# Performance work log

Hardware: AMD Instinct MI355X
Metric: run time of the kernel (lower is better)

Reference implementation:

```python
import jax, jax.numpy as jnp
import numpy as np

E = 8       # num experts
T = 1024    # num tokens
H = 1024    # hidden dim
I = 1024    # intermediate dim (per gate/up half)


def setup_inputs() -> dict:
    key = jax.random.key(0)
    k1, k2, k3, k4 = jax.random.split(key, 4)
    return {
        "hidden_states": jax.random.normal(k1, (T, H), jnp.float32),
        "router_logits": jax.random.normal(k2, (T, E), jnp.float32),
        # W13 stored pre-transposed as in the module: [E, H, 2*I]
        "W13": jax.random.normal(k3, (E, H, 2 * I), jnp.float32) * 0.02,
        # W2 stored pre-transposed: [E, I, H]
        "W2": jax.random.normal(k4, (E, I, H), jnp.float32) * 0.02,
        "top_k": 2,
    }


def reference(hidden_states, router_logits, W13, W2, top_k):
    num_experts = router_logits.shape[-1]
    # --- routing: topk_softmax (softmax over all experts, then top-k) ---
    probs = jax.nn.softmax(router_logits, axis=-1)            # [T, E]
    w, idx = jax.lax.top_k(probs, top_k)                      # [T, K]
    # renormalize=True path of moe_gather
    w = w / jnp.sum(w, axis=-1, keepdims=True)
    # combine weights per expert: [T, E]
    combine = jnp.sum(jax.nn.one_hot(idx, num_experts, dtype=w.dtype) * w[..., None], axis=1)
    # --- grouped gate-up GEMM + silu_and_mul ---
    h13 = jnp.einsum('th,ehf->tef', hidden_states, W13)       # [T, E, 2I]
    gate, up = jnp.split(h13, 2, axis=-1)                     # each [T, E, I]
    act = jax.nn.silu(gate) * up                              # silu_and_mul
    # --- grouped down GEMM ---
    down = jnp.einsum('tei,eih->teh', act, W2)                # [T, E, H]
    # --- combine (moe_gather) ---
    return jnp.einsum('te,teh->th', combine, down)            # [T, H]
```

## Files before the change

kernel.cpp:

```cpp
#include <hip/hip_runtime.h>
#include <hip/hip_bf16.h>
#include <stdint.h>

#define NE    8
#define NTOK  1024
#define NH    1024
#define NI    1024
#define N13   2048
#define NPAIR 2048

typedef __attribute__((ext_vector_type(8))) short short8;
typedef __attribute__((ext_vector_type(4))) float f32x4;
typedef unsigned short u16;
typedef unsigned int   u32;

#define WAIT_VM4 0x0F74
#define WAIT_VM3 0x0F73
#define WAIT_VM0 0x0F70

__device__ __forceinline__ u16 f2bf(float x) {
    union { float f; u32 u; } v; v.f = x;
    return (u16)((v.u + 0x7fffu + ((v.u >> 16) & 1u)) >> 16);
}

__device__ __forceinline__ void async_ld16(u16* lds, const u16* g) {
    __builtin_amdgcn_global_load_lds(
        (const __attribute__((address_space(1))) u32*)g,
        (__attribute__((address_space(3))) u32*)lds, 16, 0, 0);
}

__global__ __launch_bounds__(256) void route_kernel(
    const float* __restrict__ logits,
    int* __restrict__ counts, int* __restrict__ pair_tok,
    float* __restrict__ pair_w)
{
    __shared__ int s_cnt[NE];
    __shared__ int s_base[NE];
    const int tid = threadIdx.x;
    if (tid < NE) s_cnt[tid] = 0;
    __syncthreads();

    int eA[4][2]; int slotA[4][2]; float wA[4][2];

    #pragma unroll
    for (int i = 0; i < 4; i++) {
        const int t = tid * 4 + i;
        float l[NE];
        #pragma unroll
        for (int e = 0; e < NE; e++) l[e] = logits[t * NE + e];
        int i0 = 0;
        #pragma unroll
        for (int e = 1; e < NE; e++) if (l[e] > l[i0]) i0 = e;
        int i1 = -1;
        #pragma unroll
        for (int e = 0; e < NE; e++) {
            if (e == i0) continue;
            if (i1 < 0 || l[e] > l[i1]) i1 = e;
        }
        const float e10 = __expf(l[i1] - l[i0]);
        const float inv = 1.0f / (1.0f + e10);
        eA[i][0] = i0; eA[i][1] = i1;
        wA[i][0] = inv; wA[i][1] = e10 * inv;
        slotA[i][0] = atomicAdd(&s_cnt[i0], 1);
        slotA[i][1] = atomicAdd(&s_cnt[i1], 1);
    }
    __syncthreads();
    if (tid == 0) {
        int acc = 0;
        #pragma unroll
        for (int e = 0; e < NE; e++) { s_base[e] = acc; acc += s_cnt[e]; }
    }
    __syncthreads();
    if (tid < NE) counts[tid] = s_cnt[tid];
    #pragma unroll
    for (int i = 0; i < 4; i++) {
        const int t = tid * 4 + i;
        #pragma unroll
        for (int k = 0; k < 2; k++) {
            const int p = s_base[eA[i][k]] + slotA[i][k];
            pair_tok[p] = t;
            pair_w[p]   = wA[i][k];
        }
    }
}

__device__ __forceinline__ bool find_tile(
    const int* __restrict__ counts, int tile, int bm, int ntn,
    int& e_o, int& mt_o, int& nt_o, int& cnt_o, int& base_o)
{
    int base = 0;
    #pragma unroll
    for (int e = 0; e < NE; e++) {
        const int cnt = counts[e];
        const int mtiles = (cnt + bm - 1) / bm;
        const int tiles = mtiles * ntn;
        if (tile < tiles) {
            e_o = e; mt_o = tile / ntn; nt_o = tile - (tile / ntn) * ntn;
            cnt_o = cnt; base_o = base; return true;
        }
        tile -= tiles; base += cnt;
    }
    return false;
}

__global__ __launch_bounds__(256) void cvt_x_kernel(
    const float* __restrict__ src, u16* __restrict__ dst)
{
    const int i = blockIdx.x * 256 + threadIdx.x;
    const float4* s = (const float4*)src;
    const float4 a = s[2 * i], b = s[2 * i + 1];
    uint4 o;
    o.x = f2bf(a.x) | ((u32)f2bf(a.y) << 16);
    o.y = f2bf(a.z) | ((u32)f2bf(a.w) << 16);
    o.z = f2bf(b.x) | ((u32)f2bf(b.y) << 16);
    o.w = f2bf(b.z) | ((u32)f2bf(b.w) << 16);
    *(uint4*)(dst + (size_t)i * 8) = o;
}

__global__ __launch_bounds__(256) void cvt_tr_kernel(
    const float* __restrict__ src, u16* __restrict__ dst, int K, int N)
{
    __shared__ float Ts[64][65];
    const int ktiles = K >> 6, ntiles = N >> 6;
    const int tpe = ktiles * ntiles;
    const int e = blockIdx.x / tpe;
    const int rem = blockIdx.x - e * tpe;
    const int kt = rem / ntiles, nt = rem - (rem / ntiles) * ntiles;
    const float* sb = src + ((size_t)e * K + (size_t)kt * 64) * N + nt * 64;
    const int tid = threadIdx.x;

    #pragma unroll
    for (int i = 0; i < 4; i++) {
        const int idx = tid + i * 256;
        const int r = idx >> 4, c = (idx & 15) << 2;
        const float4 v = *(const float4*)(sb + (size_t)r * N + c);
        Ts[r][c + 0] = v.x; Ts[r][c + 1] = v.y;
        Ts[r][c + 2] = v.z; Ts[r][c + 3] = v.w;
    }
    __syncthreads();
    u16* db = dst + ((size_t)e * N + (size_t)nt * 64) * K + kt * 64;
    #pragma unroll
    for (int i = 0; i < 2; i++) {
        const int u = tid + i * 256;
        const int n = u >> 3, k8 = (u & 7) << 3;
        uint4 o;
        o.x = f2bf(Ts[k8 + 0][n]) | ((u32)f2bf(Ts[k8 + 1][n]) << 16);
        o.y = f2bf(Ts[k8 + 2][n]) | ((u32)f2bf(Ts[k8 + 3][n]) << 16);
        o.z = f2bf(Ts[k8 + 4][n]) | ((u32)f2bf(Ts[k8 + 5][n]) << 16);
        o.w = f2bf(Ts[k8 + 6][n]) | ((u32)f2bf(Ts[k8 + 7][n]) << 16);
        *(uint4*)(db + (size_t)n * K + k8) = o;
    }
}

__global__ __launch_bounds__(256) void gemm1_kernel(
    const u16* __restrict__ Xb, const u16* __restrict__ W13t,
    const int* __restrict__ counts, const int* __restrict__ pair_tok,
    u16* __restrict__ act)
{
    int e, mt, nt, cnt, base;
    if (!find_tile(counts, blockIdx.x, 128, NI / 64, e, mt, nt, cnt, base)) return;

    __shared__ u16 As[2][128 * 32];
    __shared__ u16 Bs[2][128 * 32];

    const int tid = threadIdx.x;
    const int ct  = nt * 64;

    const int m0 = tid >> 2;
    const int sw16 = (((tid & 3) ^ (m0 & 3)) << 3);
    const int t0 = pair_tok[base + min(mt * 128 + m0, cnt - 1)];
    const int t1 = pair_tok[base + min(mt * 128 + 64 + m0, cnt - 1)];
    const u16* ga0 = Xb + (size_t)t0 * NH + sw16;
    const u16* ga1 = Xb + (size_t)t1 * NH + sw16;
    const u16* gb0 = W13t + ((size_t)e * N13 + ct + m0) * 1024 + sw16;
    const u16* gb1 = W13t + ((size_t)e * N13 + NI + ct + m0) * 1024 + sw16;

    const int lane = tid & 63, w = tid >> 6;
    const int quad = lane >> 4, lid = lane & 15;
    const int rw = w >> 1, cw = w & 1;
    const int fsw = (quad ^ (lid & 3)) << 3;
    int aoff[4], bgoff[2], buoff[2];
    #pragma unroll
    for (int mi = 0; mi < 4; mi++)
        aoff[mi] = (rw * 64 + mi * 16 + lid) * 32 + fsw;
    #pragma unroll
    for (int nj = 0; nj < 2; nj++) {
        bgoff[nj] = (cw * 32 + nj * 16 + lid) * 32 + fsw;
        buoff[nj] = (64 + cw * 32 + nj * 16 + lid) * 32 + fsw;
    }

    f32x4 accg[4][2] = {};
    f32x4 accu[4][2] = {};

#define ISSUE1(b, k0)                                        \
    {                                                        \
        async_ld16(&As[b][tid * 8],         ga0 + (k0));     \
        async_ld16(&As[b][(tid + 256) * 8], ga1 + (k0));     \
        async_ld16(&Bs[b][tid * 8],         gb0 + (k0));     \
        async_ld16(&Bs[b][(tid + 256) * 8], gb1 + (k0));     \
    }
#define COMP1(b)                                                               \
    {                                                                          \
        short8 av[4], gv[2], uv[2];                                            \
        _Pragma("unroll") for (int mi = 0; mi < 4; mi++)                       \
            av[mi] = *(const short8*)&As[b][aoff[mi]];                         \
        _Pragma("unroll") for (int nj = 0; nj < 2; nj++) {                     \
            gv[nj] = *(const short8*)&Bs[b][bgoff[nj]];                        \
            uv[nj] = *(const short8*)&Bs[b][buoff[nj]];                        \
        }                                                                      \
        _Pragma("unroll") for (int mi = 0; mi < 4; mi++)                       \
            _Pragma("unroll") for (int nj = 0; nj < 2; nj++) {                 \
                accg[mi][nj] = __builtin_amdgcn_mfma_f32_16x16x32_bf16(        \
                    av[mi], gv[nj], accg[mi][nj], 0, 0, 0);                    \
                accu[mi][nj] = __builtin_amdgcn_mfma_f32_16x16x32_bf16(        \
                    av[mi], uv[nj], accu[mi][nj], 0, 0, 0);                    \
            }                                                                  \
    }

    ISSUE1(0, 0);
    int buf = 0;
    for (int k0 = 32; k0 < NH; k0 += 32) {
        ISSUE1(buf ^ 1, k0);
        __builtin_amdgcn_s_waitcnt(WAIT_VM4);
        __builtin_amdgcn_s_barrier();
        COMP1(buf);
        __builtin_amdgcn_s_barrier();
        buf ^= 1;
    }
    __builtin_amdgcn_s_waitcnt(WAIT_VM0);
    __builtin_amdgcn_s_barrier();
    COMP1(buf);

    #pragma unroll
    for (int mi = 0; mi < 4; mi++) {
        #pragma unroll
        for (int nj = 0; nj < 2; nj++) {
            const int col = ct + cw * 32 + nj * 16 + lid;
            #pragma unroll
            for (int r = 0; r < 4; r++) {
                const int row = mt * 128 + rw * 64 + mi * 16 + quad * 4 + r;
                if (row < cnt) {
                    const float g = accg[mi][nj][r], u = accu[mi][nj][r];
                    const float s = g / (1.0f + __expf(-g)) * u;
                    act[(size_t)(base + row) * NI + col] = f2bf(s);
                }
            }
        }
    }
#undef ISSUE1
#undef COMP1
}

__global__ __launch_bounds__(256) void gemm2_kernel(
    const u16* __restrict__ act, const u16* __restrict__ W2t,
    const int* __restrict__ counts, const int* __restrict__ pair_tok,
    const float* __restrict__ pair_w, float* __restrict__ out)
{
    int e, mt, nt, cnt, base;
    if (!find_tile(counts, blockIdx.x, 128, NH / 64, e, mt, nt, cnt, base)) return;

    __shared__ u16 As[2][128 * 32];
    __shared__ u16 Bs[2][64 * 32];

    const int tid = threadIdx.x;
    const int ct  = nt * 64;

    const int m0 = tid >> 2;
    const int sw16 = (((tid & 3) ^ (m0 & 3)) << 3);
    const int p0 = base + min(mt * 128 + m0, cnt - 1);
    const int p1 = base + min(mt * 128 + 64 + m0, cnt - 1);
    const u16* ga0 = act + (size_t)p0 * NI + sw16;
    const u16* ga1 = act + (size_t)p1 * NI + sw16;
    const u16* gb0 = W2t + ((size_t)e * 1024 + ct + m0) * 1024 + sw16;

    const int lane = tid & 63, w = tid >> 6;
    const int quad = lane >> 4, lid = lane & 15;
    const int rw = w >> 1, cw = w & 1;
    const int fsw = (quad ^ (lid & 3)) << 3;
    int aoff[4], boff[2];
    #pragma unroll
    for (int mi = 0; mi < 4; mi++)
        aoff[mi] = (rw * 64 + mi * 16 + lid) * 32 + fsw;
    #pragma unroll
    for (int nj = 0; nj < 2; nj++)
        boff[nj] = (cw * 32 + nj * 16 + lid) * 32 + fsw;

    f32x4 acc[4][2] = {};

#define ISSUE2(b, k0)                                        \
    {                                                        \
        async_ld16(&As[b][tid * 8],         ga0 + (k0));     \
        async_ld16(&As[b][(tid + 256) * 8], ga1 + (k0));     \
        async_ld16(&Bs[b][tid * 8],         gb0 + (k0));     \
    }
#define COMP2(b)                                                               \
    {                                                                          \
        short8 av[4], bv[2];                                                   \
        _Pragma("unroll") for (int mi = 0; mi < 4; mi++)                       \
            av[mi] = *(const short8*)&As[b][aoff[mi]];                         \
        _Pragma("unroll") for (int nj = 0; nj < 2; nj++)                       \
            bv[nj] = *(const short8*)&Bs[b][boff[nj]];                         \
        _Pragma("unroll") for (int mi = 0; mi < 4; mi++)                       \
            _Pragma("unroll") for (int nj = 0; nj < 2; nj++)                   \
                acc[mi][nj] = __builtin_amdgcn_mfma_f32_16x16x32_bf16(         \
                    av[mi], bv[nj], acc[mi][nj], 0, 0, 0);                     \
    }

    ISSUE2(0, 0);
    int buf = 0;
    for (int k0 = 32; k0 < NI; k0 += 32) {
        ISSUE2(buf ^ 1, k0);
        __builtin_amdgcn_s_waitcnt(WAIT_VM3);
        __builtin_amdgcn_s_barrier();
        COMP2(buf);
        __builtin_amdgcn_s_barrier();
        buf ^= 1;
    }
    __builtin_amdgcn_s_waitcnt(WAIT_VM0);
    __builtin_amdgcn_s_barrier();
    COMP2(buf);

    #pragma unroll
    for (int mi = 0; mi < 4; mi++) {
        #pragma unroll
        for (int r = 0; r < 4; r++) {
            const int row = mt * 128 + rw * 64 + mi * 16 + quad * 4 + r;
            if (row < cnt) {
                const int p = base + row;
                const int t = pair_tok[p];
                const float wgt = pair_w[p];
                #pragma unroll
                for (int nj = 0; nj < 2; nj++) {
                    const int col = ct + cw * 32 + nj * 16 + lid;
                    atomicAdd(out + (size_t)t * NH + col, wgt * acc[mi][nj][r]);
                }
            }
        }
    }
#undef ISSUE2
#undef COMP2
}

extern "C" void kernel_launch(void* const* d_in, const int* in_sizes, int n_in,
                              void* d_out, int out_size, void* d_ws, size_t ws_size,
                              hipStream_t stream)
{
    const float* X      = (const float*)d_in[0];
    const float* logits = (const float*)d_in[1];
    const float* W13    = (const float*)d_in[2];
    const float* W2     = (const float*)d_in[3];
    float* out = (float*)d_out;

    char* ws = (char*)d_ws;
    int*   counts   = (int*)(ws + 0);
    int*   pair_tok = (int*)(ws + 256);
    float* pair_w   = (float*)(ws + 256 + 8192);
    u16*   Xb       = (u16*)(ws + 65536);
    u16*   W13t     = (u16*)(ws + 4194304);
    u16*   W2t      = (u16*)(ws + 4194304 + 33554432);
    u16*   act      = (u16*)(ws + 54525952);

    hipMemsetAsync(d_out, 0, (size_t)NTOK * NH * sizeof(float), stream);
    route_kernel<<<1, 256, 0, stream>>>(logits, counts, pair_tok, pair_w);
    cvt_x_kernel<<<512, 256, 0, stream>>>(X, Xb);
    cvt_tr_kernel<<<NE * 16 * 32, 256, 0, stream>>>(W13, W13t, NH, N13);
    cvt_tr_kernel<<<NE * 16 * 16, 256, 0, stream>>>(W2, W2t, NI, NH);

    const int grid1 = (NPAIR / 128 + NE - 1) * (NI / 64);
    const int grid2 = (NPAIR / 128 + NE - 1) * (NH / 64);
    gemm1_kernel<<<grid1, 256, 0, stream>>>(Xb, W13t, counts, pair_tok, act);
    gemm2_kernel<<<grid2, 256, 0, stream>>>(act, W2t, counts, pair_tok, pair_w, out);
}
```

Measured before the change: 200.2 us.

## Merge prep kernels, shrink GEMM tiles for more blocks, simplify pipeline sync

Folds routing and X conversion into one kernel and merges both weight convert-transpose launches into one, cutting launch count. Halves the gemm1 N tile (32 columns of gate and up) and the gemm2 M tile (64 rows), so each GEMM launches more blocks to fill the GPU. The explicit vmcnt waits and paired barriers are replaced by a single __syncthreads at the top of each k-step, which likely drains the prefetch before compute and weakens load/compute overlap. Smaller tiles also reduce operand reuse per block.

Result: faster. 190.2 us (-5.0%).

```diff
diff --git a/kernel.cpp b/kernel.cpp
--- a/kernel.cpp
+++ b/kernel.cpp
@@ -14,10 +14,6 @@
 typedef unsigned short u16;
 typedef unsigned int   u32;
 
-#define WAIT_VM4 0x0F74
-#define WAIT_VM3 0x0F73
-#define WAIT_VM0 0x0F70
-
 __device__ __forceinline__ u16 f2bf(float x) {
     union { float f; u32 u; } v; v.f = x;
     return (u16)((v.u + 0x7fffu + ((v.u >> 16) & 1u)) >> 16);
@@ -29,14 +25,27 @@
         (__attribute__((address_space(3))) u32*)lds, 16, 0, 0);
 }
 
-__global__ __launch_bounds__(256) void route_kernel(
-    const float* __restrict__ logits,
+__global__ __launch_bounds__(256) void prep_kernel(
+    const float* __restrict__ logits, const float* __restrict__ X,
     int* __restrict__ counts, int* __restrict__ pair_tok,
-    float* __restrict__ pair_w)
-{
+    float* __restrict__ pair_w, u16* __restrict__ Xb)
+{
+    const int tid = threadIdx.x;
+    if (blockIdx.x > 0) {
+        const int i = (blockIdx.x - 1) * 256 + tid;
+        const float4* s = (const float4*)X;
+        const float4 a = s[2 * i], b = s[2 * i + 1];
+        uint4 o;
+        o.x = f2bf(a.x) | ((u32)f2bf(a.y) << 16);
+        o.y = f2bf(a.z) | ((u32)f2bf(a.w) << 16);
+        o.z = f2bf(b.x) | ((u32)f2bf(b.y) << 16);
+        o.w = f2bf(b.z) | ((u32)f2bf(b.w) << 16);
+        *(uint4*)(Xb + (size_t)i * 8) = o;
+        return;
+    }
+
     __shared__ int s_cnt[NE];
     __shared__ int s_base[NE];
-    const int tid = threadIdx.x;
     if (tid < NE) s_cnt[tid] = 0;
     __syncthreads();
 
@@ -84,47 +93,19 @@
     }
 }
 
-__device__ __forceinline__ bool find_tile(
-    const int* __restrict__ counts, int tile, int bm, int ntn,
-    int& e_o, int& mt_o, int& nt_o, int& cnt_o, int& base_o)
-{
-    int base = 0;
-    #pragma unroll
-    for (int e = 0; e < NE; e++) {
-        const int cnt = counts[e];
-        const int mtiles = (cnt + bm - 1) / bm;
-        const int tiles = mtiles * ntn;
-        if (tile < tiles) {
-            e_o = e; mt_o = tile / ntn; nt_o = tile - (tile / ntn) * ntn;
-            cnt_o = cnt; base_o = base; return true;
-        }
-        tile -= tiles; base += cnt;
-    }
-    return false;
-}
-
-__global__ __launch_bounds__(256) void cvt_x_kernel(
-    const float* __restrict__ src, u16* __restrict__ dst)
-{
-    const int i = blockIdx.x * 256 + threadIdx.x;
-    const float4* s = (const float4*)src;
-    const float4 a = s[2 * i], b = s[2 * i + 1];
-    uint4 o;
-    o.x = f2bf(a.x) | ((u32)f2bf(a.y) << 16);
-    o.y = f2bf(a.z) | ((u32)f2bf(a.w) << 16);
-    o.z = f2bf(b.x) | ((u32)f2bf(b.y) << 16);
-    o.w = f2bf(b.z) | ((u32)f2bf(b.w) << 16);
-    *(uint4*)(dst + (size_t)i * 8) = o;
-}
-
-__global__ __launch_bounds__(256) void cvt_tr_kernel(
-    const float* __restrict__ src, u16* __restrict__ dst, int K, int N)
+__global__ __launch_bounds__(256) void cvt_w_kernel(
+    const float* __restrict__ W13, u16* __restrict__ W13t,
+    const float* __restrict__ W2, u16* __restrict__ W2t)
 {
     __shared__ float Ts[64][65];
+    const float* src; u16* dst; int K, N, bid;
+    if (blockIdx.x < NE * 16 * 32) { src = W13; dst = W13t; K = NH; N = N13; bid = blockIdx.x; }
+    else                           { src = W2;  dst = W2t;  K = NI; N = NH;  bid = blockIdx.x - NE * 16 * 32; }
+
     const int ktiles = K >> 6, ntiles = N >> 6;
     const int tpe = ktiles * ntiles;
-    const int e = blockIdx.x / tpe;
-    const int rem = blockIdx.x - e * tpe;
+    const int e = bid / tpe;
+    const int rem = bid - e * tpe;
     const int kt = rem / ntiles, nt = rem - (rem / ntiles) * ntiles;
     const float* sb = src + ((size_t)e * K + (size_t)kt * 64) * N + nt * 64;
     const int tid = threadIdx.x;
@@ -152,19 +133,38 @@
     }
 }
 
+__device__ __forceinline__ bool find_tile(
+    const int* __restrict__ counts, int tile, int bm, int ntn,
+    int& e_o, int& mt_o, int& nt_o, int& cnt_o, int& base_o)
+{
+    int base = 0;
+    #pragma unroll
+    for (int e = 0; e < NE; e++) {
+        const int cnt = counts[e];
+        const int mtiles = (cnt + bm - 1) / bm;
+        const int tiles = mtiles * ntn;
+        if (tile < tiles) {
+            e_o = e; mt_o = tile / ntn; nt_o = tile - (tile / ntn) * ntn;
+            cnt_o = cnt; base_o = base; return true;
+        }
+        tile -= tiles; base += cnt;
+    }
+    return false;
+}
+
 __global__ __launch_bounds__(256) void gemm1_kernel(
     const u16* __restrict__ Xb, const u16* __restrict__ W13t,
     const int* __restrict__ counts, const int* __restrict__ pair_tok,
     u16* __restrict__ act)
 {
     int e, mt, nt, cnt, base;
-    if (!find_tile(counts, blockIdx.x, 128, NI / 64, e, mt, nt, cnt, base)) return;
+    if (!find_tile(counts, blockIdx.x, 128, NI / 32, e, mt, nt, cnt, base)) return;
 
     __shared__ u16 As[2][128 * 32];
-    __shared__ u16 Bs[2][128 * 32];
+    __shared__ u16 Bs[2][64 * 32];
 
     const int tid = threadIdx.x;
-    const int ct  = nt * 64;
+    const int ct  = nt * 32;
 
     const int m0 = tid >> 2;
     const int sw16 = (((tid & 3) ^ (m0 & 3)) << 3);
@@ -172,78 +172,65 @@
     const int t1 = pair_tok[base + min(mt * 128 + 64 + m0, cnt - 1)];
     const u16* ga0 = Xb + (size_t)t0 * NH + sw16;
     const u16* ga1 = Xb + (size_t)t1 * NH + sw16;
-    const u16* gb0 = W13t + ((size_t)e * N13 + ct + m0) * 1024 + sw16;
-    const u16* gb1 = W13t + ((size_t)e * N13 + NI + ct + m0) * 1024 + sw16;
+    const int wcol = (m0 < 32) ? (ct + m0) : (NI + ct + m0 - 32);
+    const u16* gb = W13t + ((size_t)e * N13 + wcol) * 1024 + sw16;
 
     const int lane = tid & 63, w = tid >> 6;
     const int quad = lane >> 4, lid = lane & 15;
     const int rw = w >> 1, cw = w & 1;
     const int fsw = (quad ^ (lid & 3)) << 3;
-    int aoff[4], bgoff[2], buoff[2];
+    int aoff[4];
     #pragma unroll
     for (int mi = 0; mi < 4; mi++)
         aoff[mi] = (rw * 64 + mi * 16 + lid) * 32 + fsw;
-    #pragma unroll
-    for (int nj = 0; nj < 2; nj++) {
-        bgoff[nj] = (cw * 32 + nj * 16 + lid) * 32 + fsw;
-        buoff[nj] = (64 + cw * 32 + nj * 16 + lid) * 32 + fsw;
-    }
-
-    f32x4 accg[4][2] = {};
-    f32x4 accu[4][2] = {};
+    const int bgoff = (cw * 16 + lid) * 32 + fsw;
+    const int buoff = (32 + cw * 16 + lid) * 32 + fsw;
+
+    f32x4 accg[4] = {};
+    f32x4 accu[4] = {};
 
 #define ISSUE1(b, k0)                                        \
     {                                                        \
         async_ld16(&As[b][tid * 8],         ga0 + (k0));     \
         async_ld16(&As[b][(tid + 256) * 8], ga1 + (k0));     \
-        async_ld16(&Bs[b][tid * 8],         gb0 + (k0));     \
-        async_ld16(&Bs[b][(tid + 256) * 8], gb1 + (k0));     \
+        async_ld16(&Bs[b][tid * 8],         gb  + (k0));     \
     }
 #define COMP1(b)                                                               \
     {                                                                          \
-        short8 av[4], gv[2], uv[2];                                            \
+        short8 av[4];                                                          \
         _Pragma("unroll") for (int mi = 0; mi < 4; mi++)                       \
             av[mi] = *(const short8*)&As[b][aoff[mi]];                         \
-        _Pragma("unroll") for (int nj = 0; nj < 2; nj++) {                     \
-            gv[nj] = *(const short8*)&Bs[b][bgoff[nj]];                        \
-            uv[nj] = *(const short8*)&Bs[b][buoff[nj]];                        \
+        const short8 gv = *(const short8*)&Bs[b][bgoff];                       \
+        const short8 uv = *(const short8*)&Bs[b][buoff];                       \
+        _Pragma("unroll") for (int mi = 0; mi < 4; mi++) {                     \
+            accg[mi] = __builtin_amdgcn_mfma_f32_16x16x32_bf16(                \
+                av[mi], gv, accg[mi], 0, 0, 0);                                \
+            accu[mi] = __builtin_amdgcn_mfma_f32_16x16x32_bf16(                \
+                av[mi], uv, accu[mi], 0, 0, 0);                                \
         }                                                                      \
-        _Pragma("unroll") for (int mi = 0; mi < 4; mi++)                       \
-            _Pragma("unroll") for (int nj = 0; nj < 2; nj++) {                 \
-                accg[mi][nj] = __builtin_amdgcn_mfma_f32_16x16x32_bf16(        \
-                    av[mi], gv[nj], accg[mi][nj], 0, 0, 0);                    \
-                accu[mi][nj] = __builtin_amdgcn_mfma_f32_16x16x32_bf16(        \
-                    av[mi], uv[nj], accu[mi][nj], 0, 0, 0);                    \
-            }                                                                  \
     }
 
     ISSUE1(0, 0);
     int buf = 0;
     for (int k0 = 32; k0 < NH; k0 += 32) {
+        __syncthreads();
         ISSUE1(buf ^ 1, k0);
-        __builtin_amdgcn_s_waitcnt(WAIT_VM4);
-        __builtin_amdgcn_s_barrier();
         COMP1(buf);
-        __builtin_amdgcn_s_barrier();
         buf ^= 1;
     }
-    __builtin_amdgcn_s_waitcnt(WAIT_VM0);
-    __builtin_amdgcn_s_barrier();
+    __syncthreads();
     COMP1(buf);
 
+    const int col = ct + cw * 16 + lid;
     #pragma unroll
     for (int mi = 0; mi < 4; mi++) {
         #pragma unroll
-        for (int nj = 0; nj < 2; nj++) {
-            const int col = ct + cw * 32 + nj * 16 + lid;
-            #pragma unroll
-            for (int r = 0; r < 4; r++) {
-                const int row = mt * 128 + rw * 64 + mi * 16 + quad * 4 + r;
-                if (row < cnt) {
-                    const float g = accg[mi][nj][r], u = accu[mi][nj][r];
-                    const float s = g / (1.0f + __expf(-g)) * u;
-                    act[(size_t)(base + row) * NI + col] = f2bf(s);
-                }
+        for (int r = 0; r < 4; r++) {
+            const int row = mt * 128 + rw * 64 + mi * 16 + quad * 4 + r;
+            if (row < cnt) {
+                const float g = accg[mi][r], u = accu[mi][r];
+                const float s = g / (1.0f + __expf(-g)) * u;
+                act[(size_t)(base + row) * NI + col] = f2bf(s);
             }
         }
     }
@@ -257,9 +244,9 @@
     const float* __restrict__ pair_w, float* __restrict__ out)
 {
     int e, mt, nt, cnt, base;
-    if (!find_tile(counts, blockIdx.x, 128, NH / 64, e, mt, nt, cnt, base)) return;
-
-    __shared__ u16 As[2][128 * 32];
+    if (!find_tile(counts, blockIdx.x, 64, NH / 64, e, mt, nt, cnt, base)) return;
+
+    __shared__ u16 As[2][64 * 32];
     __shared__ u16 Bs[2][64 * 32];
 
     const int tid = threadIdx.x;
@@ -267,40 +254,37 @@
 
     const int m0 = tid >> 2;
     const int sw16 = (((tid & 3) ^ (m0 & 3)) << 3);
-    const int p0 = base + min(mt * 128 + m0, cnt - 1);
-    const int p1 = base + min(mt * 128 + 64 + m0, cnt - 1);
-    const u16* ga0 = act + (size_t)p0 * NI + sw16;
-    const u16* ga1 = act + (size_t)p1 * NI + sw16;
-    const u16* gb0 = W2t + ((size_t)e * 1024 + ct + m0) * 1024 + sw16;
+    const int p0 = base + min(mt * 64 + m0, cnt - 1);
+    const u16* ga = act + (size_t)p0 * NI + sw16;
+    const u16* gb = W2t + ((size_t)e * 1024 + ct + m0) * 1024 + sw16;
 
     const int lane = tid & 63, w = tid >> 6;
     const int quad = lane >> 4, lid = lane & 15;
     const int rw = w >> 1, cw = w & 1;
     const int fsw = (quad ^ (lid & 3)) << 3;
-    int aoff[4], boff[2];
-    #pragma unroll
-    for (int mi = 0; mi < 4; mi++)
-        aoff[mi] = (rw * 64 + mi * 16 + lid) * 32 + fsw;
+    int aoff[2], boff[2];
+    #pragma unroll
+    for (int mi = 0; mi < 2; mi++)
+        aoff[mi] = (rw * 32 + mi * 16 + lid) * 32 + fsw;
     #pragma unroll
     for (int nj = 0; nj < 2; nj++)
         boff[nj] = (cw * 32 + nj * 16 + lid) * 32 + fsw;
 
-    f32x4 acc[4][2] = {};
+    f32x4 acc[2][2] = {};
 
 #define ISSUE2(b, k0)                                        \
     {                                                        \
-        async_ld16(&As[b][tid * 8],         ga0 + (k0));     \
-        async_ld16(&As[b][(tid + 256) * 8], ga1 + (k0));     \
-        async_ld16(&Bs[b][tid * 8],         gb0 + (k0));     \
+        async_ld16(&As[b][tid * 8], ga + (k0));              \
+        async_ld16(&Bs[b][tid * 8], gb + (k0));              \
     }
 #define COMP2(b)                                                               \
     {                                                                          \
-        short8 av[4], bv[2];                                                   \
-        _Pragma("unroll") for (int mi = 0; mi < 4; mi++)                       \
+        short8 av[2], bv[2];                                                   \
+        _Pragma("unroll") for (int mi = 0; mi < 2; mi++)                       \
             av[mi] = *(const short8*)&As[b][aoff[mi]];                         \
         _Pragma("unroll") for (int nj = 0; nj < 2; nj++)                       \
             bv[nj] = *(const short8*)&Bs[b][boff[nj]];                         \
-        _Pragma("unroll") for (int mi = 0; mi < 4; mi++)                       \
+        _Pragma("unroll") for (int mi = 0; mi < 2; mi++)                       \
             _Pragma("unroll") for (int nj = 0; nj < 2; nj++)                   \
                 acc[mi][nj] = __builtin_amdgcn_mfma_f32_16x16x32_bf16(         \
                     av[mi], bv[nj], acc[mi][nj], 0, 0, 0);                     \
@@ -309,22 +293,19 @@
     ISSUE2(0, 0);
     int buf = 0;
     for (int k0 = 32; k0 < NI; k0 += 32) {
+        __syncthreads();
         ISSUE2(buf ^ 1, k0);
-        __builtin_amdgcn_s_waitcnt(WAIT_VM3);
-        __builtin_amdgcn_s_barrier();
         COMP2(buf);
-        __builtin_amdgcn_s_barrier();
         buf ^= 1;
     }
-    __builtin_amdgcn_s_waitcnt(WAIT_VM0);
-    __builtin_amdgcn_s_barrier();
+    __syncthreads();
     COMP2(buf);
 
     #pragma unroll
-    for (int mi = 0; mi < 4; mi++) {
+    for (int mi = 0; mi < 2; mi++) {
         #pragma unroll
         for (int r = 0; r < 4; r++) {
-            const int row = mt * 128 + rw * 64 + mi * 16 + quad * 4 + r;
+            const int row = mt * 64 + rw * 32 + mi * 16 + quad * 4 + r;
             if (row < cnt) {
                 const int p = base + row;
                 const int t = pair_tok[p];
@@ -361,13 +342,11 @@
     u16*   act      = (u16*)(ws + 54525952);
 
     hipMemsetAsync(d_out, 0, (size_t)NTOK * NH * sizeof(float), stream);
-    route_kernel<<<1, 256, 0, stream>>>(logits, counts, pair_tok, pair_w);
-    cvt_x_kernel<<<512, 256, 0, stream>>>(X, Xb);
-    cvt_tr_kernel<<<NE * 16 * 32, 256, 0, stream>>>(W13, W13t, NH, N13);
-    cvt_tr_kernel<<<NE * 16 * 16, 256, 0, stream>>>(W2, W2t, NI, NH);
-
-    const int grid1 = (NPAIR / 128 + NE - 1) * (NI / 64);
-    const int grid2 = (NPAIR / 128 + NE - 1) * (NH / 64);
+    prep_kernel<<<513, 256, 0, stream>>>(logits, X, counts, pair_tok, pair_w, Xb);
+    cvt_w_kernel<<<NE * 16 * 32 + NE * 16 * 16, 256, 0, stream>>>(W13, W13t, W2, W2t);
+
+    const int grid1 = (NPAIR / 128 + NE - 1) * (NI / 32);
+    const int grid2 = (NPAIR / 64 + NE - 1) * (NH / 64);
     gemm1_kernel<<<grid1, 256, 0, stream>>>(Xb, W13t, counts, pair_tok, act);
     gemm2_kernel<<<grid2, 256, 0, stream>>>(act, W2t, counts, pair_tok, pair_w, out);
 }
```
